# Kernel tuning notes

Hardware: AMD Instinct MI355X
Metric: run time of the kernel (lower is better)

## Reference

```python
import jax, jax.numpy as jnp
import numpy as np
import math

# ---- module hyperparams (from init_kwargs) ----
L = 10            # number of hash-grid levels
DIM = 4           # features per level
LOG2T = 16
T = 1 << LOG2T    # hash table size per level
BASE = 16         # base resolution
PLS = 2.0         # per_level_scale
SCALE_MULTI = 0.5
HID = 64
IN_DIM = L * DIM  # 40
OUT_DIM = 13      # 1 + 12
N = 1_000_000

# growth factor b = exp((ln(finest) - ln(base)) / (L - 1)), finest = base * pls**L
B_GROWTH = math.exp((math.log(BASE * PLS ** L) - math.log(BASE)) / (L - 1))
RES = [int(math.floor(BASE * B_GROWTH ** l)) for l in range(L)]

PRIMES = np.array([1, 2654435761, 805459861], dtype=np.uint32)
# 8 corner offsets of a voxel
OFFS = np.array([[i, j, k] for i in (0, 1) for j in (0, 1) for k in (0, 1)], dtype=np.uint32)


def _hash_coords(c):
    # c: uint32 [N, 8, 3] -> int32 [N, 8] indices into table of size T
    p = jnp.asarray(PRIMES)
    h = (c[..., 0] * p[0]) ^ (c[..., 1] * p[1]) ^ (c[..., 2] * p[2])
    return (h & jnp.uint32(T - 1)).astype(jnp.int32)


def _encode(x, tables):
    # x: [N,3] in [0,1]; tables: [L, T, DIM] -> [N, DIM, L]
    offs_u = jnp.asarray(OFFS)                      # uint32 [8,3]
    offs_b = jnp.asarray(OFFS.astype(bool))         # bool   [8,3]
    feats = []
    for l in range(L):
        xs = x * RES[l]
        bottom = jnp.floor(xs)
        frac = xs - bottom                          # [N,3]
        corners = bottom.astype(jnp.uint32)[:, None, :] + offs_u[None]  # [N,8,3]
        idx = _hash_coords(corners)                 # [N,8]
        cf = tables[l][idx]                         # [N,8,DIM] gather
        # trilinear weights: prod over dims of frac (if offset==1) else (1-frac)
        w = jnp.prod(jnp.where(offs_b[None], frac[:, None, :], 1.0 - frac[:, None, :]), axis=-1)  # [N,8]
        feats.append(jnp.einsum('nc,ncd->nd', w, cf))  # [N,DIM]
    return jnp.stack(feats, axis=-1)                # [N, DIM, L]


def setup_inputs() -> dict:
    key = jax.random.key(0)
    ks = jax.random.split(key, 10)
    x = jax.random.uniform(ks[0], (N, 3), dtype=jnp.float32)
    cr = jax.random.uniform(ks[1], (N,), dtype=jnp.float32)
    tables = jax.random.uniform(ks[2], (L, T, DIM), dtype=jnp.float32, minval=-1e-4, maxval=1e-4)
    gain = math.sqrt(2.0)  # calculate_gain('relu')

    def xavier(k, fan_in, fan_out):
        a = gain * math.sqrt(6.0 / (fan_in + fan_out))
        return jax.random.uniform(k, (fan_in, fan_out), dtype=jnp.float32, minval=-a, maxval=a)

    W1 = xavier(ks[3], IN_DIM, HID)
    b1 = jnp.zeros((HID,), jnp.float32)
    W2 = xavier(ks[4], HID, HID)
    b2 = jnp.zeros((HID,), jnp.float32)
    W3 = xavier(ks[5], HID, OUT_DIM)
    b3 = jnp.zeros((OUT_DIM,), jnp.float32)
    return {"x": x, "cr": cr, "tables": tables,
            "W1": W1, "b1": b1, "W2": W2, "b2": b2, "W3": W3, "b3": b3}


def reference(x, cr, tables, W1, b1, W2, b2, W3, b3):
    enc = _encode(x, tables)                        # [N, DIM, L]
    cr_s = cr.reshape(-1) * SCALE_MULTI             # [N]
    n = jnp.arange(L, dtype=jnp.float32).reshape(1, 1, L)
    denom = PLS * 4.0 * n * cr_s[:, None, None]     # [N,1,L]
    erf_x = 1.0 / jnp.sqrt(jnp.maximum(denom, 1e-12))  # safe_div/safe_sqrt; erf(huge)=1 at n=0
    scaling = jax.lax.erf(erf_x)
    h = (enc * scaling).reshape(-1, IN_DIM)         # [N, 40]
    h = jax.nn.selu(h @ W1 + b1)
    h = jax.nn.selu(h @ W2 + b2)
    return h @ W3 + b3                              # [N, 13]
```

## Files before the change

kernel.cpp:

```cpp
#include <hip/hip_runtime.h>
#include <cmath>

typedef unsigned int uint32;
typedef __bf16 bf16;
typedef __bf16 bf16x4 __attribute__((ext_vector_type(4)));
typedef __bf16 bf16x8 __attribute__((ext_vector_type(8)));
typedef float f32x4 __attribute__((ext_vector_type(4)));

#define LVLS 10
#define TSIZE 65536
#define TMASK 65535u
#define PRIME2 2654435761u
#define PRIME3 805459861u

#define WOFF_W1 0
#define WOFF_W2 4096
#define WOFF_W3 8192
#define W_ELEMS 9216
#define DQ_OFF 18432
#define SC_OFF 18496
#define TAB_OFF_B 18560
#define TAB_ELEMS_F (LVLS * TSIZE * 4)
#define WS_NEEDED ((size_t)TAB_OFF_B + (size_t)TAB_ELEMS_F)

struct KParams { float resf[LVLS]; };

__global__ void scale_kernel(const float* __restrict__ tables, unsigned* __restrict__ scales) {
  int tid = blockIdx.x * 256 + threadIdx.x;
  int i4 = tid * 4;
  if (i4 >= TAB_ELEMS_F) return;
  float4 v = *(const float4*)(tables + i4);
  float m = fmaxf(fmaxf(fabsf(v.x), fabsf(v.y)), fmaxf(fabsf(v.z), fabsf(v.w)));
#pragma unroll
  for (int off = 32; off; off >>= 1) m = fmaxf(m, __shfl_xor(m, off, 64));
  if ((threadIdx.x & 63) == 0) {
    int l = i4 >> 18;
    atomicMax(scales + l, __float_as_uint(m));
  }
}

__global__ void quant_kernel(const float* __restrict__ W1, const float* __restrict__ W2,
                             const float* __restrict__ W3, const float* __restrict__ tables,
                             char* __restrict__ ws8, int do_tab) {
  int tid = blockIdx.x * 256 + threadIdx.x;
  bf16* wsb = (bf16*)ws8;
  if (tid < W_ELEMS) {
    float v;
    if (tid < 4096) {
      int n = tid >> 6, k = tid & 63;
      v = (k < 40) ? W1[k * 64 + n] : 0.f;
    } else if (tid < 8192) {
      int t2 = tid - 4096; int n = t2 >> 6, k = t2 & 63;
      v = W2[k * 64 + n];
    } else {
      int t3 = tid - 8192; int n = t3 >> 6, k = t3 & 63;
      v = (n < 13) ? W3[k * 13 + n] : 0.f;
    }
    wsb[tid] = (bf16)v;
  }
  const unsigned* scales = (const unsigned*)(ws8 + SC_OFF);
  if (tid < LVLS) {
    float s = __uint_as_float(scales[tid]);
    ((float*)(ws8 + DQ_OFF))[tid] = s * (1.0f / 127.0f);
  }
  if (do_tab) {
    int i4 = tid * 4;
    if (i4 < TAB_ELEMS_F) {
      float4 v = *(const float4*)(tables + i4);
      int l = i4 >> 18;
      float s = __uint_as_float(scales[l]);
      float r = (s > 0.f) ? 127.f / s : 0.f;
      int q0 = (int)rintf(fminf(fmaxf(v.x * r, -127.f), 127.f)) + 128;
      int q1 = (int)rintf(fminf(fmaxf(v.y * r, -127.f), 127.f)) + 128;
      int q2 = (int)rintf(fminf(fmaxf(v.z * r, -127.f), 127.f)) + 128;
      int q3 = (int)rintf(fminf(fmaxf(v.w * r, -127.f), 127.f)) + 128;
      unsigned p = (q0 & 0xff) | ((q1 & 0xff) << 8) | ((q2 & 0xff) << 16) | ((q3 & 0xff) << 24);
      *(unsigned*)(ws8 + TAB_OFF_B + i4) = p;
    }
  }
}

__device__ __forceinline__ float ub0(uint32 q) {
#if __has_builtin(__builtin_amdgcn_cvt_f32_ubyte0)
  return __builtin_amdgcn_cvt_f32_ubyte0(q);
#else
  return (float)(q & 0xffu);
#endif
}
__device__ __forceinline__ float ub1(uint32 q) {
#if __has_builtin(__builtin_amdgcn_cvt_f32_ubyte1)
  return __builtin_amdgcn_cvt_f32_ubyte1(q);
#else
  return (float)((q >> 8) & 0xffu);
#endif
}
__device__ __forceinline__ float ub2(uint32 q) {
#if __has_builtin(__builtin_amdgcn_cvt_f32_ubyte2)
  return __builtin_amdgcn_cvt_f32_ubyte2(q);
#else
  return (float)((q >> 16) & 0xffu);
#endif
}
__device__ __forceinline__ float ub3(uint32 q) {
#if __has_builtin(__builtin_amdgcn_cvt_f32_ubyte3)
  return __builtin_amdgcn_cvt_f32_ubyte3(q);
#else
  return (float)(q >> 24);
#endif
}

__device__ __forceinline__ float rcp_fast(float v) {
#if __has_builtin(__builtin_amdgcn_rcpf)
  return __builtin_amdgcn_rcpf(v);
#else
  return 1.0f / v;
#endif
}

__device__ __forceinline__ float erf_fast(float xv) {
  float t = rcp_fast(fmaf(0.3275911f, xv, 1.0f));
  float p = fmaf(fmaf(fmaf(fmaf(1.061405429f, t, -1.453152027f),
                           t, 1.421413741f), t, -0.284496736f), t, 0.254829592f);
  p *= t;
  float e = __expf(-xv * xv);
  return fmaf(-p, e, 1.0f);
}

__device__ __forceinline__ float selu_f(float v) {
  float neg = 1.6732632423543772f * (__expf(v) - 1.0f);
  return 1.0507009873554805f * (v > 0.f ? v : neg);
}

__device__ __forceinline__ void level_idx(float px, float py, float pz, float rs,
                                          uint32* idx, float& fx, float& fy, float& fz) {
  float xs = px * rs, ys = py * rs, zs = pz * rs;
  float bx = floorf(xs), by = floorf(ys), bz = floorf(zs);
  fx = xs - bx; fy = ys - by; fz = zs - bz;
  uint32 cx = (uint32)bx, cy = (uint32)by, cz = (uint32)bz;
  uint32 hx0 = cx, hx1 = cx + 1u;
  uint32 hy0 = cy * PRIME2, hy1 = hy0 + PRIME2;
  uint32 hz0 = cz * PRIME3, hz1 = hz0 + PRIME3;
  idx[0] = (hx0 ^ hy0 ^ hz0) & TMASK; idx[1] = (hx0 ^ hy0 ^ hz1) & TMASK;
  idx[2] = (hx0 ^ hy1 ^ hz0) & TMASK; idx[3] = (hx0 ^ hy1 ^ hz1) & TMASK;
  idx[4] = (hx1 ^ hy0 ^ hz0) & TMASK; idx[5] = (hx1 ^ hy0 ^ hz1) & TMASK;
  idx[6] = (hx1 ^ hy1 ^ hz0) & TMASK; idx[7] = (hx1 ^ hy1 ^ hz1) & TMASK;
}

__device__ __forceinline__ void gemm_stage(const bf16* __restrict__ Arow,
                                           const bf16* __restrict__ Bbase,
                                           const float* __restrict__ bvec,
                                           bf16* __restrict__ Hwr, int lr) {
  float bias[4];
#pragma unroll
  for (int nt = 0; nt < 4; ++nt) bias[nt] = bvec[nt * 16 + lr];
  f32x4 acc[4][4];
#pragma unroll
  for (int ms = 0; ms < 4; ++ms)
#pragma unroll
    for (int nt = 0; nt < 4; ++nt) {
      f32x4 a = {bias[nt], bias[nt], bias[nt], bias[nt]};
      acc[ms][nt] = a;
    }
  bf16x8 Bf[2][4];
#pragma unroll
  for (int ks = 0; ks < 2; ++ks)
#pragma unroll
    for (int nt = 0; nt < 4; ++nt)
      Bf[ks][nt] = *(const bf16x8*)(Bbase + nt * 1024 + ks * 32);
#pragma unroll
  for (int ks = 0; ks < 2; ++ks) {
    bf16x8 Af[4];
#pragma unroll
    for (int ms = 0; ms < 4; ++ms) Af[ms] = *(const bf16x8*)(Arow + ms * 1152 + ks * 32);
#pragma unroll
    for (int ms = 0; ms < 4; ++ms)
#pragma unroll
      for (int nt = 0; nt < 4; ++nt)
        acc[ms][nt] = __builtin_amdgcn_mfma_f32_16x16x32_bf16(Af[ms], Bf[ks][nt], acc[ms][nt], 0, 0, 0);
  }
#pragma unroll
  for (int ms = 0; ms < 4; ++ms)
#pragma unroll
    for (int nt = 0; nt < 4; ++nt)
#pragma unroll
      for (int r = 0; r < 4; ++r)
        Hwr[(ms * 16 + r) * 72 + nt * 16 + lr] = (bf16)selu_f(acc[ms][nt][r]);
}

template <bool TB>
__global__ __launch_bounds__(256)
void ngp_fused(const float* __restrict__ x, const float* __restrict__ cr,
               const float* __restrict__ tables, const char* __restrict__ ws8,
               const float* __restrict__ b1, const float* __restrict__ b2,
               const float* __restrict__ b3, float* __restrict__ out,
               int N, KParams kp) {
  __shared__ __align__(16) bf16 Hbuf[256 * 72];
  const int tid = threadIdx.x;
  const int n = blockIdx.x * 256 + tid;
  const int ncl = (n < N) ? n : 0;

  const float px = x[ncl * 3 + 0];
  const float py = x[ncl * 3 + 1];
  const float pz = x[ncl * 3 + 2];
  const float crv = cr[ncl];
  const float* dq = (const float*)(ws8 + DQ_OFF);

  float feat[40];
  if (TB) {
    const uint32* tb8 = (const uint32*)(ws8 + TAB_OFF_B);
    uint32 qA[8];
    float fxA, fyA, fzA;
    {
      uint32 idxA[8];
      level_idx(px, py, pz, kp.resf[0], idxA, fxA, fyA, fzA);
#pragma unroll
      for (int c = 0; c < 8; ++c) qA[c] = tb8[idxA[c]];
    }
#pragma unroll
    for (int l = 0; l < LVLS; ++l) {
      uint32 qB[8];
      float fxB, fyB, fzB;
      if (l < LVLS - 1) {
        uint32 idxB[8];
        level_idx(px, py, pz, kp.resf[l + 1], idxB, fxB, fyB, fzB);
        const uint32* base = tb8 + (l + 1) * TSIZE;
#pragma unroll
        for (int c = 0; c < 8; ++c) qB[c] = base[idxB[c]];
      }
      float wx1 = fxA, wx0 = 1.f - fxA, wy1 = fyA, wy0 = 1.f - fyA, wz1 = fzA, wz0 = 1.f - fzA;
      float wxy00 = wx0 * wy0, wxy01 = wx0 * wy1, wxy10 = wx1 * wy0, wxy11 = wx1 * wy1;
      float w[8] = {wxy00 * wz0, wxy00 * wz1, wxy01 * wz0, wxy01 * wz1,
                    wxy10 * wz0, wxy10 * wz1, wxy11 * wz0, wxy11 * wz1};
      float a0 = 0.f, a1 = 0.f, a2 = 0.f, a3 = 0.f;
#pragma unroll
      for (int c = 0; c < 8; ++c) {
        a0 = fmaf(w[c], ub0(qA[c]), a0);
        a1 = fmaf(w[c], ub1(qA[c]), a1);
        a2 = fmaf(w[c], ub2(qA[c]), a2);
        a3 = fmaf(w[c], ub3(qA[c]), a3);
      }
      float s = erf_fast(rsqrtf(fmaxf(4.0f * (float)l * crv, 1e-12f))) * dq[l];
      float off = -128.f * s;
      feat[0 * 10 + l] = fmaf(a0, s, off);
      feat[1 * 10 + l] = fmaf(a1, s, off);
      feat[2 * 10 + l] = fmaf(a2, s, off);
      feat[3 * 10 + l] = fmaf(a3, s, off);
      if (l < LVLS - 1) {
#pragma unroll
        for (int c = 0; c < 8; ++c) qA[c] = qB[c];
        fxA = fxB; fyA = fyB; fzA = fzB;
      }
    }
  } else {
#pragma unroll 1
    for (int l = 0; l < LVLS; ++l) {
      uint32 idx[8];
      float fx, fy, fz;
      level_idx(px, py, pz, kp.resf[l], idx, fx, fy, fz);
      const float4* tb = ((const float4*)tables) + l * TSIZE;
      float f[8][4];
#pragma unroll
      for (int c = 0; c < 8; ++c) {
        float4 q = tb[idx[c]];
        f[c][0] = q.x; f[c][1] = q.y; f[c][2] = q.z; f[c][3] = q.w;
      }
      float wx1 = fx, wx0 = 1.f - fx, wy1 = fy, wy0 = 1.f - fy, wz1 = fz, wz0 = 1.f - fz;
      float wxy00 = wx0 * wy0, wxy01 = wx0 * wy1, wxy10 = wx1 * wy0, wxy11 = wx1 * wy1;
      float w[8] = {wxy00 * wz0, wxy00 * wz1, wxy01 * wz0, wxy01 * wz1,
                    wxy10 * wz0, wxy10 * wz1, wxy11 * wz0, wxy11 * wz1};
      float a0 = 0.f, a1 = 0.f, a2 = 0.f, a3 = 0.f;
#pragma unroll
      for (int c = 0; c < 8; ++c) {
        a0 = fmaf(w[c], f[c][0], a0);
        a1 = fmaf(w[c], f[c][1], a1);
        a2 = fmaf(w[c], f[c][2], a2);
        a3 = fmaf(w[c], f[c][3], a3);
      }
      float s = erf_fast(rsqrtf(fmaxf(4.0f * (float)l * crv, 1e-12f)));
      feat[0 * 10 + l] = a0 * s;
      feat[1 * 10 + l] = a1 * s;
      feat[2 * 10 + l] = a2 * s;
      feat[3 * 10 + l] = a3 * s;
    }
  }

  {
    bf16* row = Hbuf + tid * 72;
#pragma unroll
    for (int c = 0; c < 5; ++c) {
      bf16x8 v;
#pragma unroll
      for (int j = 0; j < 8; ++j) v[j] = (bf16)feat[c * 8 + j];
      *(bf16x8*)(row + c * 8) = v;
    }
    bf16x8 z;
#pragma unroll
    for (int j = 0; j < 8; ++j) z[j] = (bf16)0.f;
    *(bf16x8*)(row + 40) = z;
    *(bf16x8*)(row + 48) = z;
    *(bf16x8*)(row + 56) = z;
  }
  __syncthreads();

  const int w = tid >> 6;
  const int lane = tid & 63;
  const int lr = lane & 15;
  const int quad = lane >> 4;
  const bf16* wsb = (const bf16*)ws8;

  const bf16* Arow = Hbuf + (w * 64 + lr) * 72 + quad * 8;
  bf16* Hwr = Hbuf + (w * 64 + quad * 4) * 72;

  gemm_stage(Arow, wsb + WOFF_W1 + lr * 64 + quad * 8, b1, Hwr, lr);
  __syncthreads();
  gemm_stage(Arow, wsb + WOFF_W2 + lr * 64 + quad * 8, b2, Hwr, lr);
  __syncthreads();

  f32x4 acc3[4];
  {
    float b3v = (lr < 13) ? b3[lr] : 0.f;
#pragma unroll
    for (int ms = 0; ms < 4; ++ms) {
      f32x4 a = {b3v, b3v, b3v, b3v};
      acc3[ms] = a;
    }
    const bf16* B3b = wsb + WOFF_W3 + lr * 64 + quad * 8;
    bf16x8 B3[2];
    B3[0] = *(const bf16x8*)(B3b);
    B3[1] = *(const bf16x8*)(B3b + 32);
#pragma unroll
    for (int ks = 0; ks < 2; ++ks) {
      bf16x8 Af[4];
#pragma unroll
      for (int ms = 0; ms < 4; ++ms) Af[ms] = *(const bf16x8*)(Arow + ms * 1152 + ks * 32);
#pragma unroll
      for (int ms = 0; ms < 4; ++ms)
        acc3[ms] = __builtin_amdgcn_mfma_f32_16x16x32_bf16(Af[ms], B3[ks], acc3[ms], 0, 0, 0);
    }
  }
  __syncthreads();
  float* ob = (float*)Hbuf;
  if (lr < 13) {
#pragma unroll
    for (int ms = 0; ms < 4; ++ms)
#pragma unroll
      for (int r = 0; r < 4; ++r)
        ob[(w * 64 + quad * 4 + ms * 16 + r) * 13 + lr] = acc3[ms][r];
  }
  __syncthreads();
  const int base = blockIdx.x * (256 * 13);
  if ((blockIdx.x + 1) * 256 <= N) {
    const float4* obv = (const float4*)ob;
    float4* og = (float4*)(out + base);
#pragma unroll
    for (int i = tid; i < 832; i += 256) og[i] = obv[i];
  } else {
    const int lim = N * 13 - base;
    for (int i = tid; i < 256 * 13; i += 256)
      if (i < lim) out[base + i] = ob[i];
  }
}

extern "C" void kernel_launch(void* const* d_in, const int* in_sizes, int n_in,
                              void* d_out, int out_size, void* d_ws, size_t ws_size,
                              hipStream_t stream) {
  const float* x      = (const float*)d_in[0];
  const float* cr     = (const float*)d_in[1];
  const float* tables = (const float*)d_in[2];
  const float* W1     = (const float*)d_in[3];
  const float* b1     = (const float*)d_in[4];
  const float* W2     = (const float*)d_in[5];
  const float* b2     = (const float*)d_in[6];
  const float* W3     = (const float*)d_in[7];
  const float* b3     = (const float*)d_in[8];
  float* out = (float*)d_out;
  const int N = in_sizes[1];

  KParams kp;
  double B = exp((log(16.0 * pow(2.0, 10.0)) - log(16.0)) / 9.0);
  for (int l = 0; l < LVLS; ++l) kp.resf[l] = (float)floor(16.0 * pow(B, (double)l));

  char* ws8 = (char*)d_ws;
  const bool tb = ws_size >= WS_NEEDED;

  const int qblocks = (TAB_ELEMS_F / 4 + 255) / 256;
  if (tb) {
    (void)hipMemsetAsync(ws8 + SC_OFF, 0, 64, stream);
    scale_kernel<<<qblocks, 256, 0, stream>>>(tables, (unsigned*)(ws8 + SC_OFF));
    quant_kernel<<<qblocks, 256, 0, stream>>>(W1, W2, W3, tables, ws8, 1);
  } else {
    quant_kernel<<<(W_ELEMS + 255) / 256, 256, 0, stream>>>(W1, W2, W3, tables, ws8, 0);
  }

  int blocks = (N + 255) / 256;
  if (tb)
    ngp_fused<true><<<blocks, 256, 0, stream>>>(x, cr, tables, ws8, b1, b2, b3, out, N, kp);
  else
    ngp_fused<false><<<blocks, 256, 0, stream>>>(x, cr, tables, ws8, b1, b2, b3, out, N, kp);
}
```

Baseline: 563.8 us.

## Split fused kernel into separate encode and MLP kernels via workspace

```diff
diff --git a/kernel.cpp b/kernel.cpp
--- a/kernel.cpp
+++ b/kernel.cpp
@@ -21,7 +21,9 @@
 #define SC_OFF 18496
 #define TAB_OFF_B 18560
 #define TAB_ELEMS_F (LVLS * TSIZE * 4)
-#define WS_NEEDED ((size_t)TAB_OFF_B + (size_t)TAB_ELEMS_F)
+#define WS_TAB_NEEDED ((size_t)TAB_OFF_B + (size_t)TAB_ELEMS_F)
+#define FEAT_OFF 2640128
+#define FEAT_BLK_BYTES 20480
 
 struct KParams { float resf[LVLS]; };
 
@@ -146,6 +148,56 @@
   idx[6] = (hx1 ^ hy1 ^ hz0) & TMASK; idx[7] = (hx1 ^ hy1 ^ hz1) & TMASK;
 }
 
+__global__ __launch_bounds__(256, 6)
+void ngp_encode(const float* __restrict__ x, const float* __restrict__ cr,
+                char* __restrict__ ws8, int N, KParams kp) {
+  const int tid = threadIdx.x;
+  const int n = blockIdx.x * 256 + tid;
+  const int ncl = (n < N) ? n : 0;
+
+  const float px = x[ncl * 3 + 0];
+  const float py = x[ncl * 3 + 1];
+  const float pz = x[ncl * 3 + 2];
+  const float crv = cr[ncl];
+  const float* dq = (const float*)(ws8 + DQ_OFF);
+  const uint32* tb8 = (const uint32*)(ws8 + TAB_OFF_B);
+
+  bf16x8 f[5];
+#pragma unroll
+  for (int l = 0; l < LVLS; ++l) {
+    uint32 idx[8];
+    float fx, fy, fz;
+    level_idx(px, py, pz, kp.resf[l], idx, fx, fy, fz);
+    const uint32* base = tb8 + l * TSIZE;
+    uint32 q[8];
+#pragma unroll
+    for (int c = 0; c < 8; ++c) q[c] = base[idx[c]];
+    float wx1 = fx, wx0 = 1.f - fx, wy1 = fy, wy0 = 1.f - fy, wz1 = fz, wz0 = 1.f - fz;
+    float wxy00 = wx0 * wy0, wxy01 = wx0 * wy1, wxy10 = wx1 * wy0, wxy11 = wx1 * wy1;
+    float w[8] = {wxy00 * wz0, wxy00 * wz1, wxy01 * wz0, wxy01 * wz1,
+                  wxy10 * wz0, wxy10 * wz1, wxy11 * wz0, wxy11 * wz1};
+    float a0 = 0.f, a1 = 0.f, a2 = 0.f, a3 = 0.f;
+#pragma unroll
+    for (int c = 0; c < 8; ++c) {
+      a0 = fmaf(w[c], ub0(q[c]), a0);
+      a1 = fmaf(w[c], ub1(q[c]), a1);
+      a2 = fmaf(w[c], ub2(q[c]), a2);
+      a3 = fmaf(w[c], ub3(q[c]), a3);
+    }
+    float s = erf_fast(rsqrtf(fmaxf(4.0f * (float)l * crv, 1e-12f))) * dq[l];
+    float off = -128.f * s;
+    f[(l) >> 3][(l) & 7]           = (bf16)fmaf(a0, s, off);
+    f[(10 + l) >> 3][(10 + l) & 7] = (bf16)fmaf(a1, s, off);
+    f[(20 + l) >> 3][(20 + l) & 7] = (bf16)fmaf(a2, s, off);
+    f[(30 + l) >> 3][(30 + l) & 7] = (bf16)fmaf(a3, s, off);
+  }
+
+  char* fb = ws8 + FEAT_OFF + (size_t)blockIdx.x * FEAT_BLK_BYTES;
+#pragma unroll
+  for (int c = 0; c < 5; ++c)
+    *(bf16x8*)(fb + c * 4096 + tid * 16) = f[c];
+}
+
 __device__ __forceinline__ void gemm_stage(const bf16* __restrict__ Arow,
                                            const bf16* __restrict__ Bbase,
                                            const float* __restrict__ bvec,
@@ -185,6 +237,87 @@
 #pragma unroll
       for (int r = 0; r < 4; ++r)
         Hwr[(ms * 16 + r) * 72 + nt * 16 + lr] = (bf16)selu_f(acc[ms][nt][r]);
+}
+
+__global__ __launch_bounds__(256)
+void ngp_mlp(const char* __restrict__ ws8, const float* __restrict__ b1,
+             const float* __restrict__ b2, const float* __restrict__ b3,
+             float* __restrict__ out, int N) {
+  __shared__ __align__(16) bf16 Hbuf[256 * 72];
+  const int tid = threadIdx.x;
+
+  {
+    const char* fb = ws8 + FEAT_OFF + (size_t)blockIdx.x * FEAT_BLK_BYTES;
+    bf16* row = Hbuf + tid * 72;
+#pragma unroll
+    for (int c = 0; c < 5; ++c)
+      *(bf16x8*)(row + c * 8) = *(const bf16x8*)(fb + c * 4096 + tid * 16);
+    bf16x8 z;
+#pragma unroll
+    for (int j = 0; j < 8; ++j) z[j] = (bf16)0.f;
+    *(bf16x8*)(row + 40) = z;
+    *(bf16x8*)(row + 48) = z;
+    *(bf16x8*)(row + 56) = z;
+  }
+  __syncthreads();
+
+  const int w = tid >> 6;
+  const int lane = tid & 63;
+  const int lr = lane & 15;
+  const int quad = lane >> 4;
+  const bf16* wsb = (const bf16*)ws8;
+
+  const bf16* Arow = Hbuf + (w * 64 + lr) * 72 + quad * 8;
+  bf16* Hwr = Hbuf + (w * 64 + quad * 4) * 72;
+
+  gemm_stage(Arow, wsb + WOFF_W1 + lr * 64 + quad * 8, b1, Hwr, lr);
+  __syncthreads();
+  gemm_stage(Arow, wsb + WOFF_W2 + lr * 64 + quad * 8, b2, Hwr, lr);
+  __syncthreads();
+
+  f32x4 acc3[4];
+  {
+    float b3v = (lr < 13) ? b3[lr] : 0.f;
+#pragma unroll
+    for (int ms = 0; ms < 4; ++ms) {
+      f32x4 a = {b3v, b3v, b3v, b3v};
+      acc3[ms] = a;
+    }
+    const bf16* B3b = wsb + WOFF_W3 + lr * 64 + quad * 8;
+    bf16x8 B3[2];
+    B3[0] = *(const bf16x8*)(B3b);
+    B3[1] = *(const bf16x8*)(B3b + 32);
+#pragma unroll
+    for (int ks = 0; ks < 2; ++ks) {
+      bf16x8 Af[4];
+#pragma unroll
+      for (int ms = 0; ms < 4; ++ms) Af[ms] = *(const bf16x8*)(Arow + ms * 1152 + ks * 32);
+#pragma unroll
+      for (int ms = 0; ms < 4; ++ms)
+        acc3[ms] = __builtin_amdgcn_mfma_f32_16x16x32_bf16(Af[ms], B3[ks], acc3[ms], 0, 0, 0);
+    }
+  }
+  __syncthreads();
+  float* ob = (float*)Hbuf;
+  if (lr < 13) {
+#pragma unroll
+    for (int ms = 0; ms < 4; ++ms)
+#pragma unroll
+      for (int r = 0; r < 4; ++r)
+        ob[(w * 64 + quad * 4 + ms * 16 + r) * 13 + lr] = acc3[ms][r];
+  }
+  __syncthreads();
+  const int base = blockIdx.x * (256 * 13);
+  if ((blockIdx.x + 1) * 256 <= N) {
+    const float4* obv = (const float4*)ob;
+    float4* og = (float4*)(out + base);
+#pragma unroll
+    for (int i = tid; i < 832; i += 256) og[i] = obv[i];
+  } else {
+    const int lim = N * 13 - base;
+    for (int i = tid; i < 256 * 13; i += 256)
+      if (i < lim) out[base + i] = ob[i];
+  }
 }
 
 template <bool TB>
@@ -206,77 +339,48 @@
   const float* dq = (const float*)(ws8 + DQ_OFF);
 
   float feat[40];
-  if (TB) {
-    const uint32* tb8 = (const uint32*)(ws8 + TAB_OFF_B);
-    uint32 qA[8];
-    float fxA, fyA, fzA;
-    {
-      uint32 idxA[8];
-      level_idx(px, py, pz, kp.resf[0], idxA, fxA, fyA, fzA);
-#pragma unroll
-      for (int c = 0; c < 8; ++c) qA[c] = tb8[idxA[c]];
-    }
-#pragma unroll
-    for (int l = 0; l < LVLS; ++l) {
-      uint32 qB[8];
-      float fxB, fyB, fzB;
-      if (l < LVLS - 1) {
-        uint32 idxB[8];
-        level_idx(px, py, pz, kp.resf[l + 1], idxB, fxB, fyB, fzB);
-        const uint32* base = tb8 + (l + 1) * TSIZE;
-#pragma unroll
-        for (int c = 0; c < 8; ++c) qB[c] = base[idxB[c]];
+#pragma unroll 1
+  for (int l = 0; l < LVLS; ++l) {
+    uint32 idx[8];
+    float fx, fy, fz;
+    level_idx(px, py, pz, kp.resf[l], idx, fx, fy, fz);
+    float fv[8][4];
+    if (TB) {
+      const uint32* base = ((const uint32*)(ws8 + TAB_OFF_B)) + l * TSIZE;
+#pragma unroll
+      for (int c = 0; c < 8; ++c) {
+        uint32 q = base[idx[c]];
+        fv[c][0] = ub0(q); fv[c][1] = ub1(q); fv[c][2] = ub2(q); fv[c][3] = ub3(q);
       }
-      float wx1 = fxA, wx0 = 1.f - fxA, wy1 = fyA, wy0 = 1.f - fyA, wz1 = fzA, wz0 = 1.f - fzA;
-      float wxy00 = wx0 * wy0, wxy01 = wx0 * wy1, wxy10 = wx1 * wy0, wxy11 = wx1 * wy1;
-      float w[8] = {wxy00 * wz0, wxy00 * wz1, wxy01 * wz0, wxy01 * wz1,
-                    wxy10 * wz0, wxy10 * wz1, wxy11 * wz0, wxy11 * wz1};
-      float a0 = 0.f, a1 = 0.f, a2 = 0.f, a3 = 0.f;
+    } else {
+      const float4* tb = ((const float4*)tables) + l * TSIZE;
 #pragma unroll
       for (int c = 0; c < 8; ++c) {
-        a0 = fmaf(w[c], ub0(qA[c]), a0);
-        a1 = fmaf(w[c], ub1(qA[c]), a1);
-        a2 = fmaf(w[c], ub2(qA[c]), a2);
-        a3 = fmaf(w[c], ub3(qA[c]), a3);
+        float4 q = tb[idx[c]];
+        fv[c][0] = q.x; fv[c][1] = q.y; fv[c][2] = q.z; fv[c][3] = q.w;
       }
-      float s = erf_fast(rsqrtf(fmaxf(4.0f * (float)l * crv, 1e-12f))) * dq[l];
+    }
+    float wx1 = fx, wx0 = 1.f - fx, wy1 = fy, wy0 = 1.f - fy, wz1 = fz, wz0 = 1.f - fz;
+    float wxy00 = wx0 * wy0, wxy01 = wx0 * wy1, wxy10 = wx1 * wy0, wxy11 = wx1 * wy1;
+    float w[8] = {wxy00 * wz0, wxy00 * wz1, wxy01 * wz0, wxy01 * wz1,
+                  wxy10 * wz0, wxy10 * wz1, wxy11 * wz0, wxy11 * wz1};
+    float a0 = 0.f, a1 = 0.f, a2 = 0.f, a3 = 0.f;
+#pragma unroll
+    for (int c = 0; c < 8; ++c) {
+      a0 = fmaf(w[c], fv[c][0], a0);
+      a1 = fmaf(w[c], fv[c][1], a1);
+      a2 = fmaf(w[c], fv[c][2], a2);
+      a3 = fmaf(w[c], fv[c][3], a3);
+    }
+    float s = erf_fast(rsqrtf(fmaxf(4.0f * (float)l * crv, 1e-12f)));
+    if (TB) {
+      s *= dq[l];
       float off = -128.f * s;
       feat[0 * 10 + l] = fmaf(a0, s, off);
       feat[1 * 10 + l] = fmaf(a1, s, off);
       feat[2 * 10 + l] = fmaf(a2, s, off);
       feat[3 * 10 + l] = fmaf(a3, s, off);
-      if (l < LVLS - 1) {
-#pragma unroll
-        for (int c = 0; c < 8; ++c) qA[c] = qB[c];
-        fxA = fxB; fyA = fyB; fzA = fzB;
-      }
-    }
-  } else {
-#pragma unroll 1
-    for (int l = 0; l < LVLS; ++l) {
-      uint32 idx[8];
-      float fx, fy, fz;
-      level_idx(px, py, pz, kp.resf[l], idx, fx, fy, fz);
-      const float4* tb = ((const float4*)tables) + l * TSIZE;
-      float f[8][4];
-#pragma unroll
-      for (int c = 0; c < 8; ++c) {
-        float4 q = tb[idx[c]];
-        f[c][0] = q.x; f[c][1] = q.y; f[c][2] = q.z; f[c][3] = q.w;
-      }
-      float wx1 = fx, wx0 = 1.f - fx, wy1 = fy, wy0 = 1.f - fy, wz1 = fz, wz0 = 1.f - fz;
-      float wxy00 = wx0 * wy0, wxy01 = wx0 * wy1, wxy10 = wx1 * wy0, wxy11 = wx1 * wy1;
-      float w[8] = {wxy00 * wz0, wxy00 * wz1, wxy01 * wz0, wxy01 * wz1,
-                    wxy10 * wz0, wxy10 * wz1, wxy11 * wz0, wxy11 * wz1};
-      float a0 = 0.f, a1 = 0.f, a2 = 0.f, a3 = 0.f;
-#pragma unroll
-      for (int c = 0; c < 8; ++c) {
-        a0 = fmaf(w[c], f[c][0], a0);
-        a1 = fmaf(w[c], f[c][1], a1);
-        a2 = fmaf(w[c], f[c][2], a2);
-        a3 = fmaf(w[c], f[c][3], a3);
-      }
-      float s = erf_fast(rsqrtf(fmaxf(4.0f * (float)l * crv, 1e-12f)));
+    } else {
       feat[0 * 10 + l] = a0 * s;
       feat[1 * 10 + l] = a1 * s;
       feat[2 * 10 + l] = a2 * s;
@@ -381,7 +485,9 @@
   for (int l = 0; l < LVLS; ++l) kp.resf[l] = (float)floor(16.0 * pow(B, (double)l));
 
   char* ws8 = (char*)d_ws;
-  const bool tb = ws_size >= WS_NEEDED;
+  const int nblk = (N + 255) / 256;
+  const bool tb = ws_size >= WS_TAB_NEEDED;
+  const bool split = ws_size >= (size_t)FEAT_OFF + (size_t)nblk * FEAT_BLK_BYTES;
 
   const int qblocks = (TAB_ELEMS_F / 4 + 255) / 256;
   if (tb) {
@@ -392,9 +498,12 @@
     quant_kernel<<<(W_ELEMS + 255) / 256, 256, 0, stream>>>(W1, W2, W3, tables, ws8, 0);
   }
 
-  int blocks = (N + 255) / 256;
-  if (tb)
-    ngp_fused<true><<<blocks, 256, 0, stream>>>(x, cr, tables, ws8, b1, b2, b3, out, N, kp);
-  else
-    ngp_fused<false><<<blocks, 256, 0, stream>>>(x, cr, tables, ws8, b1, b2, b3, out, N, kp);
-}
+  if (split) {
+    ngp_encode<<<nblk, 256, 0, stream>>>(x, cr, ws8, N, kp);
+    ngp_mlp<<<nblk, 256, 0, stream>>>(ws8, b1, b2, b3, out, N);
+  } else if (tb) {
+    ngp_fused<true><<<nblk, 256, 0, stream>>>(x, cr, tables, ws8, b1, b2, b3, out, N, kp);
+  } else {
+    ngp_fused<false><<<nblk, 256, 0, stream>>>(x, cr, tables, ws8, b1, b2, b3, out, N, kp);
+  }
+}
```

Measured after the change: 544.5 us. 3.4% less time.
